# Performance work log

Measured on AMD Instinct MI355X. Metric: run time of the kernel, lower is better.

## Reference

```python
import jax, jax.numpy as jnp
import numpy as np

D = 512; E = 8; TOPK = 2; F = 2048; H = 4
SF_LEVELS = 4; SF_BASE = 4.0; LN_EPS = 1e-5


def _ln(h, s, b):
    mu = jnp.mean(h, axis=-1, keepdims=True)
    var = jnp.mean((h - mu) ** 2, axis=-1, keepdims=True)
    return (h - mu) / jnp.sqrt(var + LN_EPS) * s + b


def setup_inputs() -> dict:
    key = jax.random.key(0)
    ks = jax.random.split(key, 16)
    sc = 0.02
    inp = {
        "x": jax.random.normal(ks[0], (4, 1024, D), jnp.float32),
        "gate_w": jax.random.normal(ks[1], (D, E), jnp.float32) * sc,
        "gate_b": jnp.zeros((E,), jnp.float32),
        "ln1_s": jnp.ones((E, D), jnp.float32),
        "ln1_b": jnp.zeros((E, D), jnp.float32),
        "ln2_s": jnp.ones((E, D), jnp.float32),
        "ln2_b": jnp.zeros((E, D), jnp.float32),
        "wq": jax.random.normal(ks[2], (E, D, D), jnp.float32) * sc,
        "wk": jax.random.normal(ks[3], (E, D, D), jnp.float32) * sc,
        "wv": jax.random.normal(ks[4], (E, D, D), jnp.float32) * sc,
        "wo": jax.random.normal(ks[5], (E, D, D), jnp.float32) * sc,
        "bq": jnp.zeros((E, D), jnp.float32),
        "bk": jnp.zeros((E, D), jnp.float32),
        "bv": jnp.zeros((E, D), jnp.float32),
        "bo": jnp.zeros((E, D), jnp.float32),
        "w1": jax.random.normal(ks[6], (E, D, F), jnp.float32) * sc,
        "b1": jnp.zeros((E, F), jnp.float32),
        "w2": jax.random.normal(ks[7], (E, F, D), jnp.float32) * sc,
        "b2": jnp.zeros((E, D), jnp.float32),
    }
    return inp


def reference(x, gate_w, gate_b, ln1_s, ln1_b, ln2_s, ln2_b, wq, wk, wv, wo, bq, bk, bv, bo, w1, b1, w2, b2):
    B, S, d = x.shape
    dh = d // H
    # --- SpikingRouter ---
    logits = x @ gate_w + gate_b                       # [B,S,E]
    _, idx = jax.lax.top_k(logits, TOPK)               # [B,S,k]
    in_topk = jnp.sum(jax.nn.one_hot(idx, E, dtype=logits.dtype), axis=-2) > 0
    routing_in = jnp.where(in_topk, jax.nn.relu(logits), 0.0)
    # Scale-and-Fire neuron: multi-level threshold quantization
    mem = routing_in
    rw = jnp.zeros_like(mem)
    for lvl in range(SF_LEVELS):
        thr = SF_BASE / (2.0 ** lvl)
        spk = (mem >= thr).astype(mem.dtype)
        rw = rw + spk * thr
        mem = mem - spk * thr
    # --- all experts (SFormerBlock, post-norm transformer block) ---
    def block(p):
        l1s, l1b, l2s, l2b, Wq, Wk, Wv, Wo, Bq, Bk, Bv, Bo, W1, B1, W2, B2 = p
        q = (x @ Wq + Bq).reshape(B, S, H, dh)
        k = (x @ Wk + Bk).reshape(B, S, H, dh)
        v = (x @ Wv + Bv).reshape(B, S, H, dh)
        scores = jnp.einsum('bqhd,bkhd->bhqk', q, k) / jnp.sqrt(jnp.asarray(dh, x.dtype))
        att = jax.nn.softmax(scores, axis=-1)
        o = jnp.einsum('bhqk,bkhd->bqhd', att, v).reshape(B, S, d) @ Wo + Bo
        h = _ln(x + o, l1s, l1b)
        f = jax.nn.relu(h @ W1 + B1) @ W2 + B2
        return _ln(h + f, l2s, l2b)

    expert_outs = jax.vmap(block)((ln1_s, ln1_b, ln2_s, ln2_b, wq, wk, wv, wo, bq, bk, bv, bo, w1, b1, w2, b2))  # [E,B,S,D]
    final = jnp.einsum('ebsd,bse->bsd', expert_outs, rw)
    return final, logits
```

## Files before the change

### kernel.cpp

```cpp
#include <hip/hip_runtime.h>
#include <hip/hip_bf16.h>
#include <stdint.h>

using u16 = unsigned short;
typedef float floatx4 __attribute__((ext_vector_type(4)));
typedef __bf16 bfv8 __attribute__((ext_vector_type(8)));

#define AS1 __attribute__((address_space(1)))
#define AS3 __attribute__((address_space(3)))

__device__ __forceinline__ u16 f2bf_bits(float f) {
    __hip_bfloat16 h = __float2bfloat16(f);
    u16 u;
    __builtin_memcpy(&u, &h, 2);
    return u;
}
__device__ __forceinline__ float bf_bits2f(u16 u) {
    __hip_bfloat16 h;
    __builtin_memcpy(&h, &u, 2);
    return __bfloat162float(h);
}
__device__ __forceinline__ void gload_lds16(const void* g, void* l) {
    __builtin_amdgcn_global_load_lds((AS1 void*)(uintptr_t)g, (AS3 void*)l, 16, 0, 0);
}

__device__ __forceinline__ void stage64(const u16* __restrict__ Abase, long lda, const long* arow,
                                        const u16* __restrict__ Bb, long ldb, int k0, int tid,
                                        u16* Ad, u16* Bd) {
    #pragma unroll
    for (int j = 0; j < 4; ++j) {
        const int q   = j * 256 + tid;
        const int row = q >> 3;
        const int cg  = (q & 7) ^ (row & 7);
        gload_lds16(Abase + arow[j] * lda + k0 + cg * 8, Ad + q * 8);
        gload_lds16(Bb + (long)row * ldb + k0 + cg * 8, Bd + q * 8);
    }
}
__device__ __forceinline__ void stage_one(const u16* __restrict__ base, long ld, int tid, u16* dst) {
    #pragma unroll
    for (int j = 0; j < 4; ++j) {
        const int q   = j * 256 + tid;
        const int row = q >> 3;
        const int cg  = (q & 7) ^ (row & 7);
        gload_lds16(base + (long)row * ld + cg * 8, dst + q * 8);
    }
}
__device__ __forceinline__ void compute64(const u16* Ab, const u16* Bb, int wy, int wx,
                                          int quad, int mrow, floatx4 acc[4][4]) {
    #pragma unroll
    for (int kk = 0; kk < 2; ++kk) {
        bfv8 af[4], bf[4];
        #pragma unroll
        for (int mi = 0; mi < 4; mi++) {
            const int r = wy * 64 + mi * 16 + mrow;
            const int slot = (kk * 4 + quad) ^ (r & 7);
            af[mi] = *(const bfv8*)&Ab[r * 64 + slot * 8];
        }
        #pragma unroll
        for (int ni = 0; ni < 4; ni++) {
            const int r = wx * 64 + ni * 16 + mrow;
            const int slot = (kk * 4 + quad) ^ (r & 7);
            bf[ni] = *(const bfv8*)&Bb[r * 64 + slot * 8];
        }
        #pragma unroll
        for (int mi = 0; mi < 4; mi++)
            #pragma unroll
            for (int ni = 0; ni < 4; ni++)
                acc[mi][ni] = __builtin_amdgcn_mfma_f32_16x16x32_bf16(af[mi], bf[ni], acc[mi][ni], 0, 0, 0);
    }
}
__device__ __forceinline__ void computeQK(const u16* Kb, const bfv8 qf[2][4], int wy,
                                          int quad, int mrow, floatx4 acc[4][4]) {
    #pragma unroll
    for (int kk = 0; kk < 2; ++kk) {
        bfv8 af[4];
        #pragma unroll
        for (int mi = 0; mi < 4; mi++) {
            const int r = wy * 64 + mi * 16 + mrow;
            const int slot = (kk * 4 + quad) ^ (r & 7);
            af[mi] = *(const bfv8*)&Kb[r * 64 + slot * 8];
        }
        #pragma unroll
        for (int mi = 0; mi < 4; mi++)
            #pragma unroll
            for (int ni = 0; ni < 4; ni++)
                acc[mi][ni] = __builtin_amdgcn_mfma_f32_16x16x32_bf16(af[mi], qf[kk][ni], acc[mi][ni], 0, 0, 0);
    }
}

__global__ void cast_bf16_kernel(const float* __restrict__ in, u16* __restrict__ out, int n4,
                                 const float* __restrict__ bq, const float* __restrict__ bk,
                                 const float* __restrict__ bv, float* __restrict__ pb) {
    if (blockIdx.x >= 2048) {
        int j = (blockIdx.x - 2048) * 256 + threadIdx.x;
        const float* s = j < 4096 ? bq : (j < 8192 ? bk : bv);
        pb[j] = s[j & 4095];
        return;
    }
    int i = blockIdx.x * blockDim.x + threadIdx.x;
    if (i >= n4) return;
    float4 v = ((const float4*)in)[i];
    ushort4 o;
    o.x = f2bf_bits(v.x); o.y = f2bf_bits(v.y); o.z = f2bf_bits(v.z); o.w = f2bf_bits(v.w);
    ((ushort4*)out)[i] = o;
}

__global__ void transpose_cast_kernel(const float* __restrict__ src, u16* __restrict__ dst,
                                      int R, int C, long sSrc, long sDst) {
    __shared__ float tile[32][33];
    const float* s = src + (long)blockIdx.z * sSrc;
    u16* d = dst + (long)blockIdx.z * sDst;
    int c0 = blockIdx.x * 32, r0 = blockIdx.y * 32;
    int tx = threadIdx.x, ty = threadIdx.y;
    #pragma unroll
    for (int i = 0; i < 4; i++)
        tile[ty + 8*i][tx] = s[(long)(r0 + ty + 8*i) * C + c0 + tx];
    __syncthreads();
    #pragma unroll
    for (int i = 0; i < 4; i++)
        d[(long)(c0 + ty + 8*i) * R + r0 + tx] = f2bf_bits(tile[tx][ty + 8*i]);
}

__global__ void transpose_cast4_kernel(const float* __restrict__ w0, const float* __restrict__ w1p,
                                       const float* __restrict__ w2p, const float* __restrict__ w3p,
                                       u16* __restrict__ dst) {
    __shared__ float tile[32][33];
    int z = blockIdx.z;
    const float* s = (z < 8 ? w0 : z < 16 ? w1p : z < 24 ? w2p : w3p) + (long)(z & 7) * 262144;
    u16* d = dst + (long)z * 262144;
    int c0 = blockIdx.x * 32, r0 = blockIdx.y * 32;
    int tx = threadIdx.x, ty = threadIdx.y;
    #pragma unroll
    for (int i = 0; i < 4; i++)
        tile[ty + 8*i][tx] = s[(long)(r0 + ty + 8*i) * 512 + c0 + tx];
    __syncthreads();
    #pragma unroll
    for (int i = 0; i < 4; i++)
        d[(long)(c0 + ty + 8*i) * 512 + r0 + tx] = f2bf_bits(tile[tx][ty + 8*i]);
}

__global__ __launch_bounds__(512)
void router_kernel(const float* __restrict__ x, const float* __restrict__ gw,
                   const float* __restrict__ gb, float* __restrict__ rw,
                   float* __restrict__ logits_out) {
    int row = blockIdx.x;
    int w = threadIdx.x >> 6;
    int lane = threadIdx.x & 63;
    const float* xr = x + (long)row * 512;
    float sum = 0.f;
    #pragma unroll
    for (int i = 0; i < 8; i++) {
        int d = lane + 64 * i;
        sum += xr[d] * gw[d * 8 + w];
    }
    #pragma unroll
    for (int o = 32; o; o >>= 1) sum += __shfl_down(sum, o, 64);
    __shared__ float lg[8];
    if (lane == 0) lg[w] = sum + gb[w];
    __syncthreads();
    if (threadIdx.x == 0) {
        float l[8];
        #pragma unroll
        for (int e = 0; e < 8; e++) l[e] = lg[e];
        int i1 = 0;
        for (int e = 1; e < 8; e++) if (l[e] > l[i1]) i1 = e;
        int i2 = -1;
        for (int e = 0; e < 8; e++) { if (e == i1) continue; if (i2 < 0 || l[e] > l[i2]) i2 = e; }
        for (int e = 0; e < 8; e++) {
            float v = (e == i1 || e == i2) ? (l[e] > 0.f ? l[e] : 0.f) : 0.f;
            float r = 0.f, mem = v;
            #pragma unroll
            for (int lvl = 0; lvl < 4; lvl++) {
                float thr = 4.0f / (float)(1 << lvl);
                if (mem >= thr) { r += thr; mem -= thr; }
            }
            rw[(long)row * 8 + e] = r;
            logits_out[(long)row * 8 + e] = l[e];
        }
    }
}

__global__ __launch_bounds__(256)
void build_lists_kernel(const float* __restrict__ rw, int* __restrict__ prix,
                        int* __restrict__ act, int* __restrict__ smap,
                        int* __restrict__ tmap, int* __restrict__ tt, int* __restrict__ pt) {
    int b = blockIdx.x;
    int t = threadIdx.x, wv = t >> 6, lane = t & 63;
    __shared__ int wsum[4];
    __shared__ int base_sh;
    if (t == 0) base_sh = 0;
    __syncthreads();
    for (int e = 0; e < 8; e++) {
        int r0 = b * 1024 + t * 4;
        int f[4], c = 0;
        #pragma unroll
        for (int i = 0; i < 4; i++) {
            f[i] = (rw[(long)(r0 + i) * 8 + e] != 0.f) ? 1 : 0;
            c += f[i];
        }
        int incl = c;
        #pragma unroll
        for (int o = 1; o < 64; o <<= 1) {
            int n = __shfl_up(incl, o, 64);
            if (lane >= o) incl += n;
        }
        if (lane == 63) wsum[wv] = incl;
        __syncthreads();
        int woff = 0;
        #pragma unroll
        for (int k = 0; k < 4; k++) if (k < wv) woff += wsum[k];
        int tot = wsum[0] + wsum[1] + wsum[2] + wsum[3];
        int excl = incl - c + woff;
        int base = base_sh;
        int slot = excl;
        #pragma unroll
        for (int i = 0; i < 4; i++) {
            int r = r0 + i;
            if (f[i]) {
                int ps = base + slot;
                prix[b * 3072 + ps] = r;
                act[b * 3072 + ps] = 1;
                smap[(long)r * 8 + e] = ps;
                slot++;
            } else {
                smap[(long)r * 8 + e] = -1;
            }
        }
        int pad = (tot + 127) & ~127;
        for (int s = tot + t; s < pad; s += 256) {
            prix[b * 3072 + base + s] = b * 1024;
            act[b * 3072 + base + s] = 0;
        }
        for (int k = t; k < (pad >> 7); k += 256)
            tmap[b * 32 + (base >> 7) + k] = e;
        __syncthreads();
        if (t == 0) base_sh = base + pad;
        __syncthreads();
    }
    if (t == 0) {
        tt[b] = base_sh >> 7;
        pt[b] = base_sh;
    }
}

template<bool TRANSC>
__global__ __launch_bounds__(256)
void gemm_dense_kernel(const u16* __restrict__ A,
                       const u16* __restrict__ B, long sB,
                       u16* __restrict__ C, long sC,
                       const float* __restrict__ bias, int K) {
    __shared__ __align__(16) u16 As[2][128 * 64];
    __shared__ __align__(16) u16 Bs[2][128 * 64];
    const int z = blockIdx.z;
    const u16* Bb = B + (long)z * sB + (long)blockIdx.x * 128 * 512;

    const int tid = threadIdx.x;
    const int w = tid >> 6, lane = tid & 63;
    const int wy = w >> 1, wx = w & 1;
    const int quad = lane >> 4, mrow = lane & 15;

    long arow[4];
    #pragma unroll
    for (int j = 0; j < 4; ++j) arow[j] = (long)blockIdx.y * 128 + ((j * 256 + tid) >> 3);

    floatx4 acc[4][4];
    #pragma unroll
    for (int i = 0; i < 4; i++)
        #pragma unroll
        for (int j = 0; j < 4; j++)
            acc[i][j] = floatx4{0.f, 0.f, 0.f, 0.f};

    const int nk = K >> 6;
    stage64(A, 512, arow, Bb, 512, 0, tid, As[0], Bs[0]);
    for (int it = 0; it < nk; ++it) {
        const int cur = it & 1;
        __syncthreads();
        if (it + 1 < nk)
            stage64(A, 512, arow, Bb, 512, (it + 1) << 6, tid, As[1 - cur], Bs[1 - cur]);
        compute64(As[cur], Bs[cur], wy, wx, quad, mrow, acc);
    }

    const float* biasb = bias + (long)z * 512 + blockIdx.x * 128;
    if constexpr (TRANSC) {
        u16* Cb = C + (long)z * sC;
        #pragma unroll
        for (int ni = 0; ni < 4; ni++) {
            const int colt = wx * 64 + ni * 16 + mrow;
            const int n = blockIdx.x * 128 + colt;
            float bv = biasb[colt];
            #pragma unroll
            for (int mi = 0; mi < 4; mi++) {
                #pragma unroll
                for (int r = 0; r < 4; r++) {
                    const int m = blockIdx.y * 128 + wy * 64 + mi * 16 + quad * 4 + r;
                    float v = acc[mi][ni][r] + bv;
                    long addr = ((long)(((m >> 10) << 2) + (n >> 7)) * 128 + (n & 127)) * 1024 + (m & 1023);
                    Cb[addr] = f2bf_bits(v);
                }
            }
        }
    } else {
        u16* Cb = C + (long)z * sC + (long)blockIdx.y * 128 * 512 + blockIdx.x * 128;
        #pragma unroll
        for (int ni = 0; ni < 4; ni++) {
            const int col = wx * 64 + ni * 16 + mrow;
            float bv = biasb[col];
            #pragma unroll
            for (int mi = 0; mi < 4; mi++) {
                #pragma unroll
                for (int r = 0; r < 4; r++) {
                    const int row = wy * 64 + mi * 16 + quad * 4 + r;
                    Cb[(long)row * 512 + col] = f2bf_bits(acc[mi][ni][r] + bv);
                }
            }
        }
    }
}

__global__ __launch_bounds__(256, 2)
void attn_fused_kernel(const u16* __restrict__ QP, const u16* __restrict__ Km,
                       const u16* __restrict__ VT, u16* __restrict__ OC,
                       const int* __restrict__ tmap, const int* __restrict__ tt, float alpha) {
    const int tile = blockIdx.x;
    const int bh = blockIdx.y;
    const int b = bh >> 2, h = bh & 3;
    if (tile >= tt[b]) return;
    const int e = tmap[b * 32 + tile];

    __shared__ __align__(16) u16 Bs[2][128 * 64];
    __shared__ __align__(16) u16 Ps[2][128 * 64];
    __shared__ float rs_sh[2][128];

    const int tid = threadIdx.x;
    const int w = tid >> 6, lane = tid & 63;
    const int wy = w >> 1, wx = w & 1;
    const int quad = lane >> 4, mrow = lane & 15;

    const u16* Qbase = QP + ((long)b * 3072 + tile * 128) * 512 + h * 128;
    const u16* Kbase = Km + ((long)e * 4096 + b * 1024) * 512 + h * 128;
    const u16* Vbase = VT + ((long)e * 16 + bh) * 131072;

    stage_one(Qbase, 512, tid, Ps[0]);
    stage_one(Qbase + 64, 512, tid, Ps[1]);
    __syncthreads();
    bfv8 qf[2][2][4];
    #pragma unroll
    for (int c = 0; c < 2; c++)
        #pragma unroll
        for (int kk = 0; kk < 2; kk++)
            #pragma unroll
            for (int ni = 0; ni < 4; ni++) {
                const int r = wx * 64 + ni * 16 + mrow;
                const int slot = (kk * 4 + quad) ^ (r & 7);
                qf[c][kk][ni] = *(const bfv8*)&Ps[c][r * 64 + slot * 8];
            }

    floatx4 acc_o[4][4];
    float rsum[4];
    #pragma unroll
    for (int i = 0; i < 4; i++) {
        rsum[i] = 0.f;
        #pragma unroll
        for (int j = 0; j < 4; j++) acc_o[i][j] = floatx4{0.f, 0.f, 0.f, 0.f};
    }

    for (int kt = 0; kt < 8; ++kt) {
        __syncthreads();
        stage_one(Kbase + (long)kt * 128 * 512,      512, tid, Bs[0]);
        stage_one(Kbase + (long)kt * 128 * 512 + 64, 512, tid, Bs[1]);
        __syncthreads();

        floatx4 acc_s[4][4];
        #pragma unroll
        for (int i = 0; i < 4; i++)
            #pragma unroll
            for (int j = 0; j < 4; j++) acc_s[i][j] = floatx4{0.f, 0.f, 0.f, 0.f};
        computeQK(Bs[0], qf[0], wy, quad, mrow, acc_s);
        computeQK(Bs[1], qf[1], wy, quad, mrow, acc_s);

        #pragma unroll
        for (int mi = 0; mi < 4; mi++)
            #pragma unroll
            for (int ni = 0; ni < 4; ni++)
                #pragma unroll
                for (int r = 0; r < 4; r++) {
                    float p = __expf(acc_s[mi][ni][r] * alpha);
                    acc_s[mi][ni][r] = p;
                    rsum[ni] += p;
                }

        __syncthreads();
        stage_one(Vbase + kt * 128,      1024, tid, Bs[0]);
        stage_one(Vbase + kt * 128 + 64, 1024, tid, Bs[1]);
        u16* Pw = Ps[wy];
        #pragma unroll
        for (int mi = 0; mi < 4; mi++) {
            const int sb = mi * 2 + (quad >> 1);
            #pragma unroll
            for (int ni = 0; ni < 4; ni++) {
                const int q = wx * 64 + ni * 16 + mrow;
                u16* pr = Pw + q * 64 + (sb ^ (q & 7)) * 8 + (quad & 1) * 4;
                #pragma unroll
                for (int r = 0; r < 4; r += 2) {
                    uint32_t pk = (uint32_t)f2bf_bits(acc_s[mi][ni][r]) |
                                  ((uint32_t)f2bf_bits(acc_s[mi][ni][r + 1]) << 16);
                    *(uint32_t*)(pr + r) = pk;
                }
            }
        }
        __syncthreads();
        compute64(Bs[0], Ps[0], wy, wx, quad, mrow, acc_o);
        compute64(Bs[1], Ps[1], wy, wx, quad, mrow, acc_o);
    }

    #pragma unroll
    for (int ni = 0; ni < 4; ni++) {
        float v = rsum[ni];
        v += __shfl_xor(v, 16, 64);
        v += __shfl_xor(v, 32, 64);
        if (quad == 0) rs_sh[wy][wx * 64 + ni * 16 + mrow] = v;
    }
    __syncthreads();
    u16* Cb = OC + ((long)b * 3072 + tile * 128) * 512 + h * 128;
    #pragma unroll
    for (int ni = 0; ni < 4; ni++) {
        const int q = wx * 64 + ni * 16 + mrow;
        const float inv = 1.f / (rs_sh[0][q] + rs_sh[1][q]);
        #pragma unroll
        for (int mi = 0; mi < 4; mi++) {
            ushort4 st;
            st.x = f2bf_bits(acc_o[mi][ni][0] * inv);
            st.y = f2bf_bits(acc_o[mi][ni][1] * inv);
            st.z = f2bf_bits(acc_o[mi][ni][2] * inv);
            st.w = f2bf_bits(acc_o[mi][ni][3] * inv);
            *(ushort4*)(Cb + (long)q * 512 + wy * 64 + mi * 16 + quad * 4) = st;
        }
    }
}

template<bool RELU, bool GATHER>
__global__ __launch_bounds__(256)
void gemm_packed_kernel(const u16* __restrict__ A, int lda,
                        const u16* __restrict__ B, int ldb, long sBe,
                        u16* __restrict__ C, int ldc,
                        const float* __restrict__ bias, long sBiasE,
                        const int* __restrict__ tmap, const int* __restrict__ tt, int K,
                        const int* __restrict__ prix) {
    const int b = blockIdx.y / 24, tile = blockIdx.y % 24;
    if (tile >= tt[b]) return;
    const int e = tmap[b * 32 + tile];
    __shared__ __align__(16) u16 As[2][128 * 64];
    __shared__ __align__(16) u16 Bs[2][128 * 64];
    const long rbase = (long)b * 3072 + tile * 128;
    const u16* Ab = GATHER ? A : A + rbase * lda;
    const u16* Bb = B + (long)e * sBe + (long)blockIdx.x * 128 * ldb;

    const int tid = threadIdx.x;
    const int w = tid >> 6, lane = tid & 63;
    const int wy = w >> 1, wx = w & 1;
    const int quad = lane >> 4, mrow = lane & 15;

    long arow[4];
    #pragma unroll
    for (int j = 0; j < 4; ++j) {
        const int lr = (j * 256 + tid) >> 3;
        arow[j] = GATHER ? (long)prix[b * 3072 + tile * 128 + lr] : (long)lr;
    }

    floatx4 acc[4][4];
    #pragma unroll
    for (int i = 0; i < 4; i++)
        #pragma unroll
        for (int j = 0; j < 4; j++)
            acc[i][j] = floatx4{0.f, 0.f, 0.f, 0.f};

    const int nk = K >> 6;
    stage64(Ab, lda, arow, Bb, ldb, 0, tid, As[0], Bs[0]);
    for (int it = 0; it < nk; ++it) {
        const int cur = it & 1;
        __syncthreads();
        if (it + 1 < nk)
            stage64(Ab, lda, arow, Bb, ldb, (it + 1) << 6, tid, As[1 - cur], Bs[1 - cur]);
        compute64(As[cur], Bs[cur], wy, wx, quad, mrow, acc);
    }

    u16* Cb = C + rbase * ldc + (long)blockIdx.x * 128;
    const float* biasb = bias + (long)e * sBiasE + blockIdx.x * 128;
    #pragma unroll
    for (int ni = 0; ni < 4; ni++) {
        const int col = wx * 64 + ni * 16 + mrow;
        float bv = biasb[col];
        #pragma unroll
        for (int mi = 0; mi < 4; mi++) {
            #pragma unroll
            for (int r = 0; r < 4; r++) {
                const int row = wy * 64 + mi * 16 + quad * 4 + r;
                float v = acc[mi][ni][r] + bv;
                if (RELU) v = fmaxf(v, 0.f);
                Cb[(long)row * ldc + col] = f2bf_bits(v);
            }
        }
    }
}

__global__ __launch_bounds__(128)
void ln1_kernel(const float* __restrict__ x, const u16* __restrict__ tc,
                const int* __restrict__ prix, const int* __restrict__ act,
                const int* __restrict__ tmap, const int* __restrict__ pt,
                const float* __restrict__ s_all, const float* __restrict__ b_all,
                u16* __restrict__ hb) {
    int blk = blockIdx.x;
    int b = blk / 3072, pslot = blk % 3072;
    if (pslot >= pt[b]) return;
    long row = (long)b * 3072 + pslot;
    int tid = threadIdx.x, w = tid >> 6, lane = tid & 63;
    if (!act[row]) {
        *(ushort4*)(hb + row * 512 + tid * 4) = make_ushort4(0, 0, 0, 0);
        return;
    }
    int r = prix[row];
    int e = tmap[b * 32 + (pslot >> 7)];
    float4 xv = *(const float4*)(x + (long)r * 512 + tid * 4);
    ushort4 tu = *(const ushort4*)(tc + row * 512 + tid * 4);
    float v[4] = {xv.x + bf_bits2f(tu.x), xv.y + bf_bits2f(tu.y),
                  xv.z + bf_bits2f(tu.z), xv.w + bf_bits2f(tu.w)};
    float sum = v[0] + v[1] + v[2] + v[3];
    #pragma unroll
    for (int o = 32; o; o >>= 1) sum += __shfl_down(sum, o, 64);
    __shared__ float sh[4];
    if (lane == 0) sh[w] = sum;
    __syncthreads();
    float mu = (sh[0] + sh[1]) * (1.f / 512.f);
    float sq = 0.f;
    #pragma unroll
    for (int j = 0; j < 4; j++) { float d = v[j] - mu; sq += d * d; }
    #pragma unroll
    for (int o = 32; o; o >>= 1) sq += __shfl_down(sq, o, 64);
    if (lane == 0) sh[2 + w] = sq;
    __syncthreads();
    float inv = 1.f / sqrtf((sh[2] + sh[3]) * (1.f / 512.f) + 1e-5f);
    float4 sv = *(const float4*)(s_all + e * 512 + tid * 4);
    float4 bv = *(const float4*)(b_all + e * 512 + tid * 4);
    ushort4 ub;
    ub.x = f2bf_bits((v[0] - mu) * inv * sv.x + bv.x);
    ub.y = f2bf_bits((v[1] - mu) * inv * sv.y + bv.y);
    ub.z = f2bf_bits((v[2] - mu) * inv * sv.z + bv.z);
    ub.w = f2bf_bits((v[3] - mu) * inv * sv.w + bv.w);
    *(ushort4*)(hb + row * 512 + tid * 4) = ub;
}

__global__ __launch_bounds__(128)
void ln2acc_kernel(const u16* __restrict__ hb, const u16* __restrict__ t2,
                   const float* __restrict__ s_all, const float* __restrict__ b_all,
                   const float* __restrict__ rw, const int* __restrict__ smap,
                   float* __restrict__ out) {
    long r = blockIdx.x;
    int b = (int)(r >> 10);
    int tid = threadIdx.x, w = tid >> 6, lane = tid & 63;
    __shared__ float sh[4];
    float4 acc = make_float4(0.f, 0.f, 0.f, 0.f);
    for (int e = 0; e < 8; e++) {
        int ps = smap[r * 8 + e];
        if (ps >= 0) {
            float wgt = rw[r * 8 + e];
            long row = (long)b * 3072 + ps;
            ushort4 hu = *(const ushort4*)(hb + row * 512 + tid * 4);
            ushort4 fu = *(const ushort4*)(t2 + row * 512 + tid * 4);
            float v[4] = {bf_bits2f(hu.x) + bf_bits2f(fu.x), bf_bits2f(hu.y) + bf_bits2f(fu.y),
                          bf_bits2f(hu.z) + bf_bits2f(fu.z), bf_bits2f(hu.w) + bf_bits2f(fu.w)};
            float sum = v[0] + v[1] + v[2] + v[3];
            #pragma unroll
            for (int o = 32; o; o >>= 1) sum += __shfl_down(sum, o, 64);
            if (lane == 0) sh[w] = sum;
            __syncthreads();
            float mu = (sh[0] + sh[1]) * (1.f / 512.f);
            float sq = 0.f;
            #pragma unroll
            for (int j = 0; j < 4; j++) { float d = v[j] - mu; sq += d * d; }
            #pragma unroll
            for (int o = 32; o; o >>= 1) sq += __shfl_down(sq, o, 64);
            if (lane == 0) sh[2 + w] = sq;
            __syncthreads();
            float inv = 1.f / sqrtf((sh[2] + sh[3]) * (1.f / 512.f) + 1e-5f);
            float4 sv = *(const float4*)(s_all + e * 512 + tid * 4);
            float4 bv = *(const float4*)(b_all + e * 512 + tid * 4);
            acc.x += wgt * ((v[0] - mu) * inv * sv.x + bv.x);
            acc.y += wgt * ((v[1] - mu) * inv * sv.y + bv.y);
            acc.z += wgt * ((v[2] - mu) * inv * sv.z + bv.z);
            acc.w += wgt * ((v[3] - mu) * inv * sv.w + bv.w);
            __syncthreads();
        }
    }
    *(float4*)(out + r * 512 + tid * 4) = acc;
}

static const size_t WB_B   = 0;
static const size_t RW_B   = 50331648;
static const size_t PB_B   = 50462720;
static const size_t TT_B   = 50511872;
static const size_t PT_B   = 50511888;
static const size_t TMAP_B = 50511904;
static const size_t PRIX_B = 50512416;
static const size_t ACT_B  = 50561568;
static const size_t SMAP_B = 50610720;
static const size_t XB_B   = 50741792;
static const size_t Q8_B   = 54936096;
static const size_t K8_B   = 88490528;
static const size_t VT_B   = 122044960;
static const size_t S_B    = 155599392;
static const size_t OC_B   = Q8_B;
static const size_t TC_B   = K8_B;
static const size_t HB_B   = Q8_B;
static const size_t MID_B  = S_B;
static const size_t T2_B   = VT_B;

extern "C" void kernel_launch(void* const* d_in, const int* in_sizes, int n_in,
                              void* d_out, int out_size, void* d_ws, size_t ws_size,
                              hipStream_t stream) {
    const float* x      = (const float*)d_in[0];
    const float* gate_w = (const float*)d_in[1];
    const float* gate_b = (const float*)d_in[2];
    const float* ln1_s  = (const float*)d_in[3];
    const float* ln1_b  = (const float*)d_in[4];
    const float* ln2_s  = (const float*)d_in[5];
    const float* ln2_b  = (const float*)d_in[6];
    const float* wq = (const float*)d_in[7];
    const float* wk = (const float*)d_in[8];
    const float* wv = (const float*)d_in[9];
    const float* wo = (const float*)d_in[10];
    const float* bo = (const float*)d_in[14];
    const float* w1 = (const float*)d_in[15];
    const float* b1 = (const float*)d_in[16];
    const float* w2 = (const float*)d_in[17];
    const float* b2 = (const float*)d_in[18];
    float* out = (float*)d_out;

    char* ws = (char*)d_ws;
    u16*   WB   = (u16*)(ws + WB_B);
    float* RW   = (float*)(ws + RW_B);
    float* PB   = (float*)(ws + PB_B);
    int*   TT   = (int*)(ws + TT_B);
    int*   PT   = (int*)(ws + PT_B);
    int*   TMAP = (int*)(ws + TMAP_B);
    int*   PRIX = (int*)(ws + PRIX_B);
    int*   ACT  = (int*)(ws + ACT_B);
    int*   SMAP = (int*)(ws + SMAP_B);
    u16*   XB   = (u16*)(ws + XB_B);
    u16*   QP   = (u16*)(ws + Q8_B);
    u16*   K8   = (u16*)(ws + K8_B);
    u16*   VT8  = (u16*)(ws + VT_B);
    u16*   OC   = (u16*)(ws + OC_B);
    u16*   TC   = (u16*)(ws + TC_B);
    u16*   HB   = (u16*)(ws + HB_B);
    u16*   MID  = (u16*)(ws + MID_B);
    u16*   T2   = (u16*)(ws + T2_B);

    cast_bf16_kernel<<<dim3(2096), 256, 0, stream>>>(x, XB, 4096 * 512 / 4,
                                                     (const float*)d_in[11], (const float*)d_in[12],
                                                     (const float*)d_in[13], PB);
    transpose_cast4_kernel<<<dim3(16,16,32), dim3(32,8), 0, stream>>>(wq, wk, wv, wo, WB);
    transpose_cast_kernel<<<dim3(64,16,8), dim3(32,8), 0, stream>>>(w1, WB + 8388608,  512,  2048, 1048576, 1048576);
    transpose_cast_kernel<<<dim3(16,64,8), dim3(32,8), 0, stream>>>(w2, WB + 16777216, 2048, 512,  1048576, 1048576);
    router_kernel<<<4096, 512, 0, stream>>>(x, gate_w, gate_b, RW, out + 2097152);
    build_lists_kernel<<<4, 256, 0, stream>>>(RW, PRIX, ACT, SMAP, TMAP, TT, PT);

    const float isq = 0.08838834764831845f;

    gemm_dense_kernel<false><<<dim3(4,32,8), 256, 0, stream>>>(
        XB, WB + 2097152, 262144, K8, 2097152, PB + 4096, 512);
    gemm_dense_kernel<true><<<dim3(4,32,8), 256, 0, stream>>>(
        XB, WB + 4194304, 262144, VT8, 2097152, PB + 8192, 512);
    gemm_packed_kernel<false, true><<<dim3(4,96), 256, 0, stream>>>(
        XB, 512, WB, 512, 262144, QP, 512, PB, 512, TMAP, TT, 512, PRIX);

    attn_fused_kernel<<<dim3(24, 16), 256, 0, stream>>>(QP, K8, VT8, OC, TMAP, TT, isq);

    gemm_packed_kernel<false, false><<<dim3(4,96), 256, 0, stream>>>(
        OC, 512, WB + 6291456, 512, 262144, TC, 512, bo, 512, TMAP, TT, 512, nullptr);
    ln1_kernel<<<12288, 128, 0, stream>>>(x, TC, PRIX, ACT, TMAP, PT, ln1_s, ln1_b, HB);
    gemm_packed_kernel<true, false><<<dim3(16,96), 256, 0, stream>>>(
        HB, 512, WB + 8388608, 512, 1048576, MID, 2048, b1, 2048, TMAP, TT, 512, nullptr);
    gemm_packed_kernel<false, false><<<dim3(4,96), 256, 0, stream>>>(
        MID, 2048, WB + 16777216, 2048, 1048576, T2, 512, b2, 512, TMAP, TT, 2048, nullptr);
    ln2acc_kernel<<<4096, 128, 0, stream>>>(HB, T2, ln2_s, ln2_b, RW, SMAP, out);
}
```

Before: 440.8 us.

## Split attention over key halves with a separate partial-sum reduce kernel

Splits the fused attention kernel along the key dimension into two halves (blockIdx.z), so each block processes 4 of the 8 key tiles and writes unnormalized fp32 partial outputs and row sums to workspace. A new reduce kernel adds the two partials, normalizes by the combined row sum and writes the bf16 output. The aim is to double the number of attention blocks so more CUs stay busy, since the original grid was small (24x16 with early exits). The cost is extra fp32 traffic for the partials plus one more kernel launch. The split is exact only because the softmax here has no running max, so the two partial sums can simply be added.

```diff
diff --git a/kernel.cpp b/kernel.cpp
--- a/kernel.cpp
+++ b/kernel.cpp
@@ -318,11 +318,13 @@
 }
 
 __global__ __launch_bounds__(256, 2)
-void attn_fused_kernel(const u16* __restrict__ QP, const u16* __restrict__ Km,
-                       const u16* __restrict__ VT, u16* __restrict__ OC,
-                       const int* __restrict__ tmap, const int* __restrict__ tt, float alpha) {
+void attn_part_kernel(const u16* __restrict__ QP, const u16* __restrict__ Km,
+                      const u16* __restrict__ VT, float* __restrict__ Opart,
+                      float* __restrict__ rsumP,
+                      const int* __restrict__ tmap, const int* __restrict__ tt, float alpha) {
     const int tile = blockIdx.x;
     const int bh = blockIdx.y;
+    const int half = blockIdx.z;
     const int b = bh >> 2, h = bh & 3;
     if (tile >= tt[b]) return;
     const int e = tmap[b * 32 + tile];
@@ -337,8 +339,8 @@
     const int quad = lane >> 4, mrow = lane & 15;
 
     const u16* Qbase = QP + ((long)b * 3072 + tile * 128) * 512 + h * 128;
-    const u16* Kbase = Km + ((long)e * 4096 + b * 1024) * 512 + h * 128;
-    const u16* Vbase = VT + ((long)e * 16 + bh) * 131072;
+    const u16* Kbase = Km + ((long)e * 4096 + b * 1024 + half * 512) * 512 + h * 128;
+    const u16* Vbase = VT + ((long)e * 16 + bh) * 131072 + half * 512;
 
     stage_one(Qbase, 512, tid, Ps[0]);
     stage_one(Qbase + 64, 512, tid, Ps[1]);
@@ -364,7 +366,7 @@
         for (int j = 0; j < 4; j++) acc_o[i][j] = floatx4{0.f, 0.f, 0.f, 0.f};
     }
 
-    for (int kt = 0; kt < 8; ++kt) {
+    for (int kt = 0; kt < 4; ++kt) {
         __syncthreads();
         stage_one(Kbase + (long)kt * 128 * 512,      512, tid, Bs[0]);
         stage_one(Kbase + (long)kt * 128 * 512 + 64, 512, tid, Bs[1]);
@@ -421,20 +423,50 @@
         if (quad == 0) rs_sh[wy][wx * 64 + ni * 16 + mrow] = v;
     }
     __syncthreads();
-    u16* Cb = OC + ((long)b * 3072 + tile * 128) * 512 + h * 128;
+    const long pbase = ((long)bh * 24 + tile) * 2 + half;
+    if (tid < 128)
+        rsumP[pbase * 128 + tid] = rs_sh[0][tid] + rs_sh[1][tid];
+    float* Op = Opart + pbase * 16384;
     #pragma unroll
     for (int ni = 0; ni < 4; ni++) {
         const int q = wx * 64 + ni * 16 + mrow;
-        const float inv = 1.f / (rs_sh[0][q] + rs_sh[1][q]);
         #pragma unroll
         for (int mi = 0; mi < 4; mi++) {
-            ushort4 st;
-            st.x = f2bf_bits(acc_o[mi][ni][0] * inv);
-            st.y = f2bf_bits(acc_o[mi][ni][1] * inv);
-            st.z = f2bf_bits(acc_o[mi][ni][2] * inv);
-            st.w = f2bf_bits(acc_o[mi][ni][3] * inv);
-            *(ushort4*)(Cb + (long)q * 512 + wy * 64 + mi * 16 + quad * 4) = st;
-        }
+            *(float4*)(Op + (long)q * 128 + wy * 64 + mi * 16 + quad * 4) =
+                make_float4(acc_o[mi][ni][0], acc_o[mi][ni][1],
+                            acc_o[mi][ni][2], acc_o[mi][ni][3]);
+        }
+    }
+}
+
+__global__ __launch_bounds__(256)
+void attn_reduce_kernel(const float* __restrict__ Opart, const float* __restrict__ rsumP,
+                        u16* __restrict__ OC, const int* __restrict__ tt) {
+    const int tile = blockIdx.x;
+    const int bh = blockIdx.y;
+    const int b = bh >> 2, h = bh & 3;
+    if (tile >= tt[b]) return;
+    const long pbase = ((long)bh * 24 + tile) * 2;
+    const float4* p0 = (const float4*)(Opart + pbase * 16384);
+    const float4* p1 = p0 + 4096;
+    const float* r0 = rsumP + pbase * 128;
+    __shared__ float inv_sh[128];
+    const int tid = threadIdx.x;
+    if (tid < 128) inv_sh[tid] = 1.f / (r0[tid] + r0[128 + tid]);
+    __syncthreads();
+    u16* Cb = OC + ((long)b * 3072 + tile * 128) * 512 + h * 128;
+    #pragma unroll
+    for (int it = 0; it < 16; ++it) {
+        const int i = it * 256 + tid;
+        const int q = i >> 5, j = i & 31;
+        float4 a = p0[i], c = p1[i];
+        const float inv = inv_sh[q];
+        ushort4 st;
+        st.x = f2bf_bits((a.x + c.x) * inv);
+        st.y = f2bf_bits((a.y + c.y) * inv);
+        st.z = f2bf_bits((a.z + c.z) * inv);
+        st.w = f2bf_bits((a.w + c.w) * inv);
+        ((ushort4*)(Cb + (long)q * 512))[j] = st;
     }
 }
 
@@ -608,6 +640,7 @@
 static const size_t K8_B   = 88490528;
 static const size_t VT_B   = 122044960;
 static const size_t S_B    = 155599392;
+static const size_t RSUM_B = 256262688;
 static const size_t OC_B   = Q8_B;
 static const size_t TC_B   = K8_B;
 static const size_t HB_B   = Q8_B;
@@ -636,24 +669,26 @@
     float* out = (float*)d_out;
 
     char* ws = (char*)d_ws;
-    u16*   WB   = (u16*)(ws + WB_B);
-    float* RW   = (float*)(ws + RW_B);
-    float* PB   = (float*)(ws + PB_B);
-    int*   TT   = (int*)(ws + TT_B);
-    int*   PT   = (int*)(ws + PT_B);
-    int*   TMAP = (int*)(ws + TMAP_B);
-    int*   PRIX = (int*)(ws + PRIX_B);
-    int*   ACT  = (int*)(ws + ACT_B);
-    int*   SMAP = (int*)(ws + SMAP_B);
-    u16*   XB   = (u16*)(ws + XB_B);
-    u16*   QP   = (u16*)(ws + Q8_B);
-    u16*   K8   = (u16*)(ws + K8_B);
-    u16*   VT8  = (u16*)(ws + VT_B);
-    u16*   OC   = (u16*)(ws + OC_B);
-    u16*   TC   = (u16*)(ws + TC_B);
-    u16*   HB   = (u16*)(ws + HB_B);
-    u16*   MID  = (u16*)(ws + MID_B);
-    u16*   T2   = (u16*)(ws + T2_B);
+    u16*   WB    = (u16*)(ws + WB_B);
+    float* RW    = (float*)(ws + RW_B);
+    float* PB    = (float*)(ws + PB_B);
+    int*   TT    = (int*)(ws + TT_B);
+    int*   PT    = (int*)(ws + PT_B);
+    int*   TMAP  = (int*)(ws + TMAP_B);
+    int*   PRIX  = (int*)(ws + PRIX_B);
+    int*   ACT   = (int*)(ws + ACT_B);
+    int*   SMAP  = (int*)(ws + SMAP_B);
+    u16*   XB    = (u16*)(ws + XB_B);
+    u16*   QP    = (u16*)(ws + Q8_B);
+    u16*   K8    = (u16*)(ws + K8_B);
+    u16*   VT8   = (u16*)(ws + VT_B);
+    float* OPART = (float*)(ws + S_B);
+    float* RSUM  = (float*)(ws + RSUM_B);
+    u16*   OC    = (u16*)(ws + OC_B);
+    u16*   TC    = (u16*)(ws + TC_B);
+    u16*   HB    = (u16*)(ws + HB_B);
+    u16*   MID   = (u16*)(ws + MID_B);
+    u16*   T2    = (u16*)(ws + T2_B);
 
     cast_bf16_kernel<<<dim3(2096), 256, 0, stream>>>(x, XB, 4096 * 512 / 4,
                                                      (const float*)d_in[11], (const float*)d_in[12],
@@ -673,7 +708,8 @@
     gemm_packed_kernel<false, true><<<dim3(4,96), 256, 0, stream>>>(
         XB, 512, WB, 512, 262144, QP, 512, PB, 512, TMAP, TT, 512, PRIX);
 
-    attn_fused_kernel<<<dim3(24, 16), 256, 0, stream>>>(QP, K8, VT8, OC, TMAP, TT, isq);
+    attn_part_kernel<<<dim3(24, 16, 2), 256, 0, stream>>>(QP, K8, VT8, OPART, RSUM, TMAP, TT, isq);
+    attn_reduce_kernel<<<dim3(24, 16), 256, 0, stream>>>(OPART, RSUM, OC, TT);
 
     gemm_packed_kernel<false, false><<<dim3(4,96), 256, 0, stream>>>(
         OC, 512, WB + 6291456, 512, 262144, TC, 512, bo, 512, TMAP, TT, 512, nullptr);
```

After: 447.7 us. Within noise of the previous version (+1.5%).

## Restructure attention into 64-key steps with register-prefetched K/V tiles

Applied to the files above, without the earlier changes.

The fused attention loop now walks the keys in sixteen 64-row steps instead of eight 128-row steps. K and V tiles are loaded into registers ahead of time and written to swizzled LDS, so global loads overlap the QK and PV MFMA work. All Q fragments stay in registers, and the P buffer is shrunk and shared. The aim is to hide global load latency and cut LDS use per block, at the cost of more barriers per key and extra register pressure from the prefetch buffers.

```diff
diff --git a/kernel.cpp b/kernel.cpp
--- a/kernel.cpp
+++ b/kernel.cpp
@@ -36,15 +36,6 @@
         gload_lds16(Bb + (long)row * ldb + k0 + cg * 8, Bd + q * 8);
     }
 }
-__device__ __forceinline__ void stage_one(const u16* __restrict__ base, long ld, int tid, u16* dst) {
-    #pragma unroll
-    for (int j = 0; j < 4; ++j) {
-        const int q   = j * 256 + tid;
-        const int row = q >> 3;
-        const int cg  = (q & 7) ^ (row & 7);
-        gload_lds16(base + (long)row * ld + cg * 8, dst + q * 8);
-    }
-}
 __device__ __forceinline__ void compute64(const u16* Ab, const u16* Bb, int wy, int wx,
                                           int quad, int mrow, floatx4 acc[4][4]) {
     #pragma unroll
@@ -67,24 +58,6 @@
             #pragma unroll
             for (int ni = 0; ni < 4; ni++)
                 acc[mi][ni] = __builtin_amdgcn_mfma_f32_16x16x32_bf16(af[mi], bf[ni], acc[mi][ni], 0, 0, 0);
-    }
-}
-__device__ __forceinline__ void computeQK(const u16* Kb, const bfv8 qf[2][4], int wy,
-                                          int quad, int mrow, floatx4 acc[4][4]) {
-    #pragma unroll
-    for (int kk = 0; kk < 2; ++kk) {
-        bfv8 af[4];
-        #pragma unroll
-        for (int mi = 0; mi < 4; mi++) {
-            const int r = wy * 64 + mi * 16 + mrow;
-            const int slot = (kk * 4 + quad) ^ (r & 7);
-            af[mi] = *(const bfv8*)&Kb[r * 64 + slot * 8];
-        }
-        #pragma unroll
-        for (int mi = 0; mi < 4; mi++)
-            #pragma unroll
-            for (int ni = 0; ni < 4; ni++)
-                acc[mi][ni] = __builtin_amdgcn_mfma_f32_16x16x32_bf16(af[mi], qf[kk][ni], acc[mi][ni], 0, 0, 0);
     }
 }
 
@@ -327,8 +300,9 @@
     if (tile >= tt[b]) return;
     const int e = tmap[b * 32 + tile];
 
-    __shared__ __align__(16) u16 Bs[2][128 * 64];
-    __shared__ __align__(16) u16 Ps[2][128 * 64];
+    __shared__ __align__(16) u16 Kb[64 * 128];
+    __shared__ __align__(16) u16 Vb[128 * 64];
+    __shared__ __align__(16) u16 Pb[128 * 64];
     __shared__ float rs_sh[2][128];
 
     const int tid = threadIdx.x;
@@ -340,20 +314,36 @@
     const u16* Kbase = Km + ((long)e * 4096 + b * 1024) * 512 + h * 128;
     const u16* Vbase = VT + ((long)e * 16 + bh) * 131072;
 
-    stage_one(Qbase, 512, tid, Ps[0]);
-    stage_one(Qbase + 64, 512, tid, Ps[1]);
-    __syncthreads();
-    bfv8 qf[2][2][4];
-    #pragma unroll
-    for (int c = 0; c < 2; c++)
-        #pragma unroll
-        for (int kk = 0; kk < 2; kk++)
-            #pragma unroll
-            for (int ni = 0; ni < 4; ni++) {
-                const int r = wx * 64 + ni * 16 + mrow;
-                const int slot = (kk * 4 + quad) ^ (r & 7);
-                qf[c][kk][ni] = *(const bfv8*)&Ps[c][r * 64 + slot * 8];
-            }
+    const int krow[4] = { (0*256+tid)>>4, (1*256+tid)>>4, (2*256+tid)>>4, (3*256+tid)>>4 };
+    const int kc  [4] = { (0*256+tid)&15, (1*256+tid)&15, (2*256+tid)&15, (3*256+tid)&15 };
+    const int vrow[4] = { (0*256+tid)>>3, (1*256+tid)>>3, (2*256+tid)>>3, (3*256+tid)>>3 };
+    const int vc  [4] = { (0*256+tid)&7,  (1*256+tid)&7,  (2*256+tid)&7,  (3*256+tid)&7  };
+
+    float4 kreg[4], vreg[4];
+    #pragma unroll
+    for (int j = 0; j < 4; ++j)
+        kreg[j] = *(const float4*)(Kbase + (long)krow[j] * 512 + kc[j] * 8);
+
+    bfv8 qf[4][4];
+    #pragma unroll
+    for (int dh = 0; dh < 2; ++dh) {
+        #pragma unroll
+        for (int j = 0; j < 4; ++j) {
+            const int q0 = j * 256 + tid;
+            const int row = q0 >> 3, c = q0 & 7, cg = c ^ (row & 7);
+            gload_lds16(Qbase + (long)row * 512 + dh * 64 + cg * 8, Pb + q0 * 8);
+        }
+        __syncthreads();
+        #pragma unroll
+        for (int dkl = 0; dkl < 2; ++dkl)
+            #pragma unroll
+            for (int ni = 0; ni < 4; ++ni) {
+                const int q = wx * 64 + ni * 16 + mrow;
+                const int c = dkl * 4 + quad;
+                qf[dh * 2 + dkl][ni] = *(const bfv8*)&Pb[q * 64 + (c ^ (q & 7)) * 8];
+            }
+        __syncthreads();
+    }
 
     floatx4 acc_o[4][4];
     float rsum[4];
@@ -364,53 +354,91 @@
         for (int j = 0; j < 4; j++) acc_o[i][j] = floatx4{0.f, 0.f, 0.f, 0.f};
     }
 
-    for (int kt = 0; kt < 8; ++kt) {
-        __syncthreads();
-        stage_one(Kbase + (long)kt * 128 * 512,      512, tid, Bs[0]);
-        stage_one(Kbase + (long)kt * 128 * 512 + 64, 512, tid, Bs[1]);
-        __syncthreads();
-
-        floatx4 acc_s[4][4];
-        #pragma unroll
-        for (int i = 0; i < 4; i++)
+    for (int s = 0; s < 16; ++s) {
+        __syncthreads();
+        #pragma unroll
+        for (int j = 0; j < 4; ++j)
+            vreg[j] = *(const float4*)(Vbase + (long)vrow[j] * 1024 + s * 64 + vc[j] * 8);
+        #pragma unroll
+        for (int j = 0; j < 4; ++j) {
+            const int cs = (kc[j] & 8) | ((kc[j] & 7) ^ (krow[j] & 7));
+            *(float4*)(Kb + krow[j] * 128 + cs * 8) = kreg[j];
+        }
+        __syncthreads();
+
+        floatx4 acc_s[2][4];
+        #pragma unroll
+        for (int i = 0; i < 2; i++)
             #pragma unroll
             for (int j = 0; j < 4; j++) acc_s[i][j] = floatx4{0.f, 0.f, 0.f, 0.f};
-        computeQK(Bs[0], qf[0], wy, quad, mrow, acc_s);
-        computeQK(Bs[1], qf[1], wy, quad, mrow, acc_s);
-
-        #pragma unroll
-        for (int mi = 0; mi < 4; mi++)
-            #pragma unroll
-            for (int ni = 0; ni < 4; ni++)
+        #pragma unroll
+        for (int dk = 0; dk < 4; ++dk) {
+            bfv8 af[2];
+            #pragma unroll
+            for (int mi = 0; mi < 2; ++mi) {
+                const int row = wy * 32 + mi * 16 + mrow;
+                const int c = dk * 4 + quad;
+                const int cs = (c & 8) | ((c & 7) ^ (row & 7));
+                af[mi] = *(const bfv8*)&Kb[row * 128 + cs * 8];
+            }
+            #pragma unroll
+            for (int mi = 0; mi < 2; ++mi)
                 #pragma unroll
-                for (int r = 0; r < 4; r++) {
+                for (int ni = 0; ni < 4; ++ni)
+                    acc_s[mi][ni] = __builtin_amdgcn_mfma_f32_16x16x32_bf16(af[mi], qf[dk][ni], acc_s[mi][ni], 0, 0, 0);
+        }
+        #pragma unroll
+        for (int mi = 0; mi < 2; ++mi)
+            #pragma unroll
+            for (int ni = 0; ni < 4; ++ni)
+                #pragma unroll
+                for (int r = 0; r < 4; ++r) {
                     float p = __expf(acc_s[mi][ni][r] * alpha);
                     acc_s[mi][ni][r] = p;
                     rsum[ni] += p;
                 }
-
-        __syncthreads();
-        stage_one(Vbase + kt * 128,      1024, tid, Bs[0]);
-        stage_one(Vbase + kt * 128 + 64, 1024, tid, Bs[1]);
-        u16* Pw = Ps[wy];
-        #pragma unroll
-        for (int mi = 0; mi < 4; mi++) {
-            const int sb = mi * 2 + (quad >> 1);
-            #pragma unroll
-            for (int ni = 0; ni < 4; ni++) {
+        const int sn = (s < 15) ? s + 1 : 15;
+        #pragma unroll
+        for (int j = 0; j < 4; ++j)
+            kreg[j] = *(const float4*)(Kbase + (long)(sn * 64 + krow[j]) * 512 + kc[j] * 8);
+        #pragma unroll
+        for (int j = 0; j < 4; ++j)
+            *(float4*)(Vb + vrow[j] * 64 + (vc[j] ^ (vrow[j] & 7)) * 8) = vreg[j];
+        #pragma unroll
+        for (int mi = 0; mi < 2; ++mi)
+            #pragma unroll
+            for (int ni = 0; ni < 4; ++ni) {
                 const int q = wx * 64 + ni * 16 + mrow;
-                u16* pr = Pw + q * 64 + (sb ^ (q & 7)) * 8 + (quad & 1) * 4;
+                const int cc = wy * 4 + mi * 2 + (quad >> 1);
+                u16* pr = Pb + q * 64 + ((cc ^ (q & 7)) * 8) + (quad & 1) * 4;
+                uint2 pk;
+                pk.x = (uint32_t)f2bf_bits(acc_s[mi][ni][0]) | ((uint32_t)f2bf_bits(acc_s[mi][ni][1]) << 16);
+                pk.y = (uint32_t)f2bf_bits(acc_s[mi][ni][2]) | ((uint32_t)f2bf_bits(acc_s[mi][ni][3]) << 16);
+                *(uint2*)pr = pk;
+            }
+        __syncthreads();
+
+        #pragma unroll
+        for (int kw = 0; kw < 2; ++kw) {
+            bfv8 vf[4], pf[4];
+            #pragma unroll
+            for (int mi = 0; mi < 4; ++mi) {
+                const int row = wy * 64 + mi * 16 + mrow;
+                const int c = kw * 4 + quad;
+                vf[mi] = *(const bfv8*)&Vb[row * 64 + (c ^ (row & 7)) * 8];
+            }
+            #pragma unroll
+            for (int ni = 0; ni < 4; ++ni) {
+                const int q = wx * 64 + ni * 16 + mrow;
+                const int c = kw * 4 + quad;
+                pf[ni] = *(const bfv8*)&Pb[q * 64 + (c ^ (q & 7)) * 8];
+            }
+            #pragma unroll
+            for (int mi = 0; mi < 4; ++mi)
                 #pragma unroll
-                for (int r = 0; r < 4; r += 2) {
-                    uint32_t pk = (uint32_t)f2bf_bits(acc_s[mi][ni][r]) |
-                                  ((uint32_t)f2bf_bits(acc_s[mi][ni][r + 1]) << 16);
-                    *(uint32_t*)(pr + r) = pk;
-                }
-            }
-        }
-        __syncthreads();
-        compute64(Bs[0], Ps[0], wy, wx, quad, mrow, acc_o);
-        compute64(Bs[1], Ps[1], wy, wx, quad, mrow, acc_o);
+                for (int ni = 0; ni < 4; ++ni)
+                    acc_o[mi][ni] = __builtin_amdgcn_mfma_f32_16x16x32_bf16(vf[mi], pf[ni], acc_o[mi][ni], 0, 0, 0);
+        }
     }
 
     #pragma unroll
```

Result: slower. 503.4 us (+14.2%).

## Pipeline K/V loads in fused attention and merge K and V projection launches

Applied to the files above, without the earlier changes.

The attention kernel now double-buffers K tiles and gives V its own buffer. The next K tile and the current V tile are issued early, and partial vmcnt waits with raw barriers let global-to-LDS loads overlap with QK and PV compute. P stores are widened to 64-bit writes. The separate K and V projection GEMM launches are merged into one grid with z=16, which relies on the K and V weights and biases being contiguous. The larger LDS footprint drops launch bounds to one block per SM, so occupancy falls in exchange for the overlap.

```diff
diff --git a/kernel.cpp b/kernel.cpp
--- a/kernel.cpp
+++ b/kernel.cpp
@@ -243,16 +243,15 @@
     }
 }
 
-template<bool TRANSC>
 __global__ __launch_bounds__(256)
-void gemm_dense_kernel(const u16* __restrict__ A,
-                       const u16* __restrict__ B, long sB,
-                       u16* __restrict__ C, long sC,
-                       const float* __restrict__ bias, int K) {
+void gemm_kv_kernel(const u16* __restrict__ A,
+                    const u16* __restrict__ Wkv,
+                    u16* __restrict__ CK, u16* __restrict__ CV,
+                    const float* __restrict__ biasKV) {
     __shared__ __align__(16) u16 As[2][128 * 64];
     __shared__ __align__(16) u16 Bs[2][128 * 64];
     const int z = blockIdx.z;
-    const u16* Bb = B + (long)z * sB + (long)blockIdx.x * 128 * 512;
+    const u16* Bb = Wkv + (long)z * 262144 + (long)blockIdx.x * 128 * 512;
 
     const int tid = threadIdx.x;
     const int w = tid >> 6, lane = tid & 63;
@@ -270,19 +269,18 @@
         for (int j = 0; j < 4; j++)
             acc[i][j] = floatx4{0.f, 0.f, 0.f, 0.f};
 
-    const int nk = K >> 6;
     stage64(A, 512, arow, Bb, 512, 0, tid, As[0], Bs[0]);
-    for (int it = 0; it < nk; ++it) {
+    for (int it = 0; it < 8; ++it) {
         const int cur = it & 1;
         __syncthreads();
-        if (it + 1 < nk)
+        if (it + 1 < 8)
             stage64(A, 512, arow, Bb, 512, (it + 1) << 6, tid, As[1 - cur], Bs[1 - cur]);
         compute64(As[cur], Bs[cur], wy, wx, quad, mrow, acc);
     }
 
-    const float* biasb = bias + (long)z * 512 + blockIdx.x * 128;
-    if constexpr (TRANSC) {
-        u16* Cb = C + (long)z * sC;
+    const float* biasb = biasKV + (long)z * 512 + blockIdx.x * 128;
+    if (z >= 8) {
+        u16* Cb = CV + (long)(z - 8) * 2097152;
         #pragma unroll
         for (int ni = 0; ni < 4; ni++) {
             const int colt = wx * 64 + ni * 16 + mrow;
@@ -300,7 +298,7 @@
             }
         }
     } else {
-        u16* Cb = C + (long)z * sC + (long)blockIdx.y * 128 * 512 + blockIdx.x * 128;
+        u16* Cb = CK + (long)z * 2097152 + (long)blockIdx.y * 128 * 512 + blockIdx.x * 128;
         #pragma unroll
         for (int ni = 0; ni < 4; ni++) {
             const int col = wx * 64 + ni * 16 + mrow;
@@ -317,7 +315,7 @@
     }
 }
 
-__global__ __launch_bounds__(256, 2)
+__global__ __launch_bounds__(256, 1)
 void attn_fused_kernel(const u16* __restrict__ QP, const u16* __restrict__ Km,
                        const u16* __restrict__ VT, u16* __restrict__ OC,
                        const int* __restrict__ tmap, const int* __restrict__ tt, float alpha) {
@@ -327,7 +325,8 @@
     if (tile >= tt[b]) return;
     const int e = tmap[b * 32 + tile];
 
-    __shared__ __align__(16) u16 Bs[2][128 * 64];
+    __shared__ __align__(16) u16 Kb[2][128 * 128];
+    __shared__ __align__(16) u16 Vb[128 * 128];
     __shared__ __align__(16) u16 Ps[2][128 * 64];
     __shared__ float rs_sh[2][128];
 
@@ -354,6 +353,7 @@
                 const int slot = (kk * 4 + quad) ^ (r & 7);
                 qf[c][kk][ni] = *(const bfv8*)&Ps[c][r * 64 + slot * 8];
             }
+    __syncthreads();
 
     floatx4 acc_o[4][4];
     float rsum[4];
@@ -364,19 +364,25 @@
         for (int j = 0; j < 4; j++) acc_o[i][j] = floatx4{0.f, 0.f, 0.f, 0.f};
     }
 
+    stage_one(Kbase, 512, tid, Kb[0]);
+    stage_one(Kbase + 64, 512, tid, Kb[0] + 8192);
+
     for (int kt = 0; kt < 8; ++kt) {
-        __syncthreads();
-        stage_one(Kbase + (long)kt * 128 * 512,      512, tid, Bs[0]);
-        stage_one(Kbase + (long)kt * 128 * 512 + 64, 512, tid, Bs[1]);
-        __syncthreads();
-
+        asm volatile("s_waitcnt vmcnt(0) lgkmcnt(0)" ::: "memory");
+        __builtin_amdgcn_s_barrier();
+        __builtin_amdgcn_sched_barrier(0);
+
+        stage_one(Vbase + kt * 128,      1024, tid, Vb);
+        stage_one(Vbase + kt * 128 + 64, 1024, tid, Vb + 8192);
+
+        const u16* K0 = Kb[kt & 1];
         floatx4 acc_s[4][4];
         #pragma unroll
         for (int i = 0; i < 4; i++)
             #pragma unroll
             for (int j = 0; j < 4; j++) acc_s[i][j] = floatx4{0.f, 0.f, 0.f, 0.f};
-        computeQK(Bs[0], qf[0], wy, quad, mrow, acc_s);
-        computeQK(Bs[1], qf[1], wy, quad, mrow, acc_s);
+        computeQK(K0,        qf[0], wy, quad, mrow, acc_s);
+        computeQK(K0 + 8192, qf[1], wy, quad, mrow, acc_s);
 
         #pragma unroll
         for (int mi = 0; mi < 4; mi++)
@@ -389,9 +395,10 @@
                     rsum[ni] += p;
                 }
 
-        __syncthreads();
-        stage_one(Vbase + kt * 128,      1024, tid, Bs[0]);
-        stage_one(Vbase + kt * 128 + 64, 1024, tid, Bs[1]);
+        const int ktn = (kt < 7) ? kt + 1 : 7;
+        stage_one(Kbase + (long)ktn * 128 * 512,      512, tid, Kb[(kt + 1) & 1]);
+        stage_one(Kbase + (long)ktn * 128 * 512 + 64, 512, tid, Kb[(kt + 1) & 1] + 8192);
+
         u16* Pw = Ps[wy];
         #pragma unroll
         for (int mi = 0; mi < 4; mi++) {
@@ -400,19 +407,22 @@
             for (int ni = 0; ni < 4; ni++) {
                 const int q = wx * 64 + ni * 16 + mrow;
                 u16* pr = Pw + q * 64 + (sb ^ (q & 7)) * 8 + (quad & 1) * 4;
-                #pragma unroll
-                for (int r = 0; r < 4; r += 2) {
-                    uint32_t pk = (uint32_t)f2bf_bits(acc_s[mi][ni][r]) |
-                                  ((uint32_t)f2bf_bits(acc_s[mi][ni][r + 1]) << 16);
-                    *(uint32_t*)(pr + r) = pk;
-                }
+                uint2 pk;
+                pk.x = (uint32_t)f2bf_bits(acc_s[mi][ni][0]) | ((uint32_t)f2bf_bits(acc_s[mi][ni][1]) << 16);
+                pk.y = (uint32_t)f2bf_bits(acc_s[mi][ni][2]) | ((uint32_t)f2bf_bits(acc_s[mi][ni][3]) << 16);
+                *(uint2*)pr = pk;
             }
         }
-        __syncthreads();
-        compute64(Bs[0], Ps[0], wy, wx, quad, mrow, acc_o);
-        compute64(Bs[1], Ps[1], wy, wx, quad, mrow, acc_o);
-    }
-
+
+        asm volatile("s_waitcnt vmcnt(8) lgkmcnt(0)" ::: "memory");
+        __builtin_amdgcn_s_barrier();
+        __builtin_amdgcn_sched_barrier(0);
+
+        compute64(Vb,        Ps[0], wy, wx, quad, mrow, acc_o);
+        compute64(Vb + 8192, Ps[1], wy, wx, quad, mrow, acc_o);
+    }
+
+    __syncthreads();
     #pragma unroll
     for (int ni = 0; ni < 4; ni++) {
         float v = rsum[ni];
@@ -666,10 +676,7 @@
 
     const float isq = 0.08838834764831845f;
 
-    gemm_dense_kernel<false><<<dim3(4,32,8), 256, 0, stream>>>(
-        XB, WB + 2097152, 262144, K8, 2097152, PB + 4096, 512);
-    gemm_dense_kernel<true><<<dim3(4,32,8), 256, 0, stream>>>(
-        XB, WB + 4194304, 262144, VT8, 2097152, PB + 8192, 512);
+    gemm_kv_kernel<<<dim3(4,32,16), 256, 0, stream>>>(XB, WB + 2097152, K8, VT8, PB + 4096);
     gemm_packed_kernel<false, true><<<dim3(4,96), 256, 0, stream>>>(
         XB, 512, WB, 512, 262144, QP, 512, PB, 512, TMAP, TT, 512, PRIX);
 
```

Result: slower. 459.7 us (+4.3%).
